# Kernel optimization log

Hardware: AMD Instinct MI355X
Metric: run time of the kernel (lower is better)

## Reference

```python
import jax, jax.numpy as jnp
import numpy as np

N, INC, INN, OUTC, OUTN, MAXD = 16, 32, 65536, 32, 8192, 16

def setup_inputs() -> dict:
    key = jax.random.key(0)
    ks = jax.random.split(key, 7)
    x = jax.random.normal(ks[0], (N, INC, INN), jnp.float32)
    A = jax.random.randint(ks[1], (OUTN, MAXD), 0, INN, dtype=jnp.int64)
    weight = 0.2 * jax.random.normal(ks[2], (INC, INN), jnp.float32)
    # normalize=True with fixed degree MAXD -> mask = 1/maxD everywhere
    mask = jnp.ones((OUTN, MAXD, 1), jnp.float32) / MAXD
    mask_weight = 0.2 * jax.random.normal(ks[3], (OUTN, MAXD, 1), jnp.float32)
    ct_weight = jax.random.normal(ks[4], (OUTC, INC), jnp.float32) / np.sqrt(INC)
    ct_bias = 0.02 * jax.random.normal(ks[5], (OUTC,), jnp.float32)
    bias = 0.2 * jax.random.normal(ks[6], (OUTC, OUTN), jnp.float32)
    return {"x": x, "A": A, "weight": weight, "mask": mask,
            "mask_weight": mask_weight, "ct_weight": ct_weight,
            "ct_bias": ct_bias, "bias": bias}

def reference(x, A, weight, mask, mask_weight, ct_weight, ct_bias, bias):
    n, inc, inn = x.shape
    outn, maxD = A.shape
    # per-input-node channel scaling, then lay out as (inn, N*inc) feature table
    feat = (x * weight).reshape(n * inc, inn).T            # (inn, N*inc)
    emb = feat[A]                                          # (outn, maxD, N*inc) gather
    w = mask_weight * mask                                 # (outn, maxD, 1)
    pooled = (w * emb).reshape(outn, maxD, n, inc).sum(axis=1)  # (outn, N, inc)
    almost_y = jnp.einsum('onc,dc->ond', pooled, ct_weight) + ct_bias  # (outn, N, outc)
    return almost_y.transpose(1, 2, 0) + bias              # (N, outc, outn)
```

## Files before the change

### kernel.cpp

```cpp
#include <hip/hip_runtime.h>
#include <hip/hip_bf16.h>

#define NN    16
#define INC   32
#define INN   65536
#define OUTC  32
#define OUTN  8192
#define MAXD  16
#define NC    512

typedef __attribute__((ext_vector_type(8))) unsigned short ushort8;

__global__ __launch_bounds__(256) void transpose_scale_kernel(
    const float* __restrict__ x,
    const float* __restrict__ weight,
    unsigned short* __restrict__ feat)
{
    __shared__ float tile[64][65];
    const int l  = threadIdx.x;
    const int j0 = blockIdx.x * 64;
    const int r0 = blockIdx.y * 64;

    #pragma unroll
    for (int it = 0; it < 4; ++it) {
        int idx = it * 256 + l;
        int rl  = idx >> 4;
        int jj  = idx & 15;
        int r   = r0 + rl;
        int c   = r & 31;
        int j   = j0 + jj * 4;
        float4 xv = *reinterpret_cast<const float4*>(x + (size_t)r * INN + j);
        float4 wv = *reinterpret_cast<const float4*>(weight + (size_t)c * INN + j);
        tile[jj * 4 + 0][rl] = xv.x * wv.x;
        tile[jj * 4 + 1][rl] = xv.y * wv.y;
        tile[jj * 4 + 2][rl] = xv.z * wv.z;
        tile[jj * 4 + 3][rl] = xv.w * wv.w;
    }
    __syncthreads();

    #pragma unroll
    for (int p = 0; p < 2; ++p) {
        int jl = p * 32 + (l >> 3);
        int rs = (l & 7) * 8;
        ushort8 pk;
        #pragma unroll
        for (int k = 0; k < 8; ++k) {
            float v = tile[jl][rs + k];
            pk[k] = __bfloat16_as_ushort(__float2bfloat16(v));
        }
        *reinterpret_cast<ushort8*>(
            feat + (size_t)(j0 + jl) * NC + r0 + rs) = pk;
    }
}

#define OTILE 16

__global__ __launch_bounds__(256) void gather_gemm_kernel(
    const unsigned short* __restrict__ feat,
    const int*   __restrict__ A,
    const float* __restrict__ mask,
    const float* __restrict__ mw,
    const float* __restrict__ ctw,
    const float* __restrict__ ctb,
    const float* __restrict__ bias,
    float*       __restrict__ out)
{
    __shared__ float pooled[OTILE][NC];
    const int l    = threadIdx.x;
    const int wave = l >> 6;
    const int lane = l & 63;
    const int o0   = blockIdx.x * OTILE;

    const int dout = l & 31;
    float ctr[32];
    #pragma unroll
    for (int q = 0; q < 8; ++q)
        *reinterpret_cast<float4*>(&ctr[4 * q]) =
            *reinterpret_cast<const float4*>(ctw + dout * 32 + 4 * q);
    const float cb = ctb[dout];

    #pragma unroll
    for (int i = 0; i < 4; ++i) {
        const int o  = wave * 4 + i;
        const int oo = o0 + o;
        float acc[8] = {0.f, 0.f, 0.f, 0.f, 0.f, 0.f, 0.f, 0.f};
        #pragma unroll
        for (int d = 0; d < MAXD; ++d) {
            int   j = A[oo * MAXD + d] & (INN - 1);
            float w = mw[oo * MAXD + d] * mask[oo * MAXD + d];
            ushort8 p = *reinterpret_cast<const ushort8*>(
                feat + (size_t)j * NC + lane * 8);
            #pragma unroll
            for (int k = 0; k < 8; ++k)
                acc[k] += w * __uint_as_float((unsigned)p[k] << 16);
        }
        *reinterpret_cast<float4*>(&pooled[o][lane * 8]) =
            make_float4(acc[0], acc[1], acc[2], acc[3]);
        *reinterpret_cast<float4*>(&pooled[o][lane * 8 + 4]) =
            make_float4(acc[4], acc[5], acc[6], acc[7]);
    }
    __syncthreads();

    #pragma unroll
    for (int h = 0; h < 2; ++h) {
        const int n = (l >> 5) + 8 * h;
        float vals[OTILE];
        #pragma unroll
        for (int o = 0; o < OTILE; ++o) {
            float s = cb;
            #pragma unroll
            for (int q = 0; q < 8; ++q) {
                float4 pv = *reinterpret_cast<const float4*>(
                    &pooled[o][n * 32 + 4 * q]);
                s += pv.x * ctr[4 * q + 0] + pv.y * ctr[4 * q + 1]
                   + pv.z * ctr[4 * q + 2] + pv.w * ctr[4 * q + 3];
            }
            vals[o] = s + bias[(size_t)dout * OUTN + o0 + o];
        }
        float4* outp = reinterpret_cast<float4*>(
            out + ((size_t)(n * 32 + dout)) * OUTN + o0);
        #pragma unroll
        for (int q = 0; q < 4; ++q)
            outp[q] = make_float4(vals[4*q], vals[4*q+1], vals[4*q+2], vals[4*q+3]);
    }
}

extern "C" void kernel_launch(void* const* d_in, const int* in_sizes, int n_in,
                              void* d_out, int out_size, void* d_ws, size_t ws_size,
                              hipStream_t stream)
{
    const float* x      = (const float*)d_in[0];
    const int*   A      = (const int*)  d_in[1];
    const float* weight = (const float*)d_in[2];
    const float* mask   = (const float*)d_in[3];
    const float* mw     = (const float*)d_in[4];
    const float* ctw    = (const float*)d_in[5];
    const float* ctb    = (const float*)d_in[6];
    const float* bias   = (const float*)d_in[7];
    float* out = (float*)d_out;

    unsigned short* feat = (unsigned short*)d_ws;

    dim3 gA(INN / 64, NC / 64);
    transpose_scale_kernel<<<gA, 256, 0, stream>>>(x, weight, feat);

    gather_gemm_kernel<<<OUTN / OTILE, 256, 0, stream>>>(
        feat, A, mask, mw, ctw, ctb, bias, out);
}
```

Baseline: 258.7 us.

## Use 512-thread gather blocks with LDS-staged indices, bias, and nontemporal I/O

The gather/GEMM kernel now runs 512 threads per block. Each wave pools two output nodes instead of four, and the neighbour indices, weights and bias tile are staged in LDS. The pooled buffer uses a permuted channel layout so each thread computes all 16 outputs for a single batch row with one pass over ct_weight, and the thread no longer holds 32 ct_weight registers. Nontemporal load/store hints are added for the streaming x reads and the output writes. The aim is more parallelism and fewer redundant global loads, in exchange for an extra barrier and possible LDS bank-conflict changes.

```diff
diff --git a/kernel.cpp b/kernel.cpp
--- a/kernel.cpp
+++ b/kernel.cpp
@@ -10,6 +10,7 @@
 #define NC    512
 
 typedef __attribute__((ext_vector_type(8))) unsigned short ushort8;
+typedef __attribute__((ext_vector_type(4))) float f32x4;
 
 __global__ __launch_bounds__(256) void transpose_scale_kernel(
     const float* __restrict__ x,
@@ -29,12 +30,13 @@
         int r   = r0 + rl;
         int c   = r & 31;
         int j   = j0 + jj * 4;
-        float4 xv = *reinterpret_cast<const float4*>(x + (size_t)r * INN + j);
-        float4 wv = *reinterpret_cast<const float4*>(weight + (size_t)c * INN + j);
-        tile[jj * 4 + 0][rl] = xv.x * wv.x;
-        tile[jj * 4 + 1][rl] = xv.y * wv.y;
-        tile[jj * 4 + 2][rl] = xv.z * wv.z;
-        tile[jj * 4 + 3][rl] = xv.w * wv.w;
+        f32x4 xv = __builtin_nontemporal_load(
+            reinterpret_cast<const f32x4*>(x + (size_t)r * INN + j));
+        f32x4 wv = *reinterpret_cast<const f32x4*>(weight + (size_t)c * INN + j);
+        tile[jj * 4 + 0][rl] = xv[0] * wv[0];
+        tile[jj * 4 + 1][rl] = xv[1] * wv[1];
+        tile[jj * 4 + 2][rl] = xv[2] * wv[2];
+        tile[jj * 4 + 3][rl] = xv[3] * wv[3];
     }
     __syncthreads();
 
@@ -55,7 +57,7 @@
 
 #define OTILE 16
 
-__global__ __launch_bounds__(256) void gather_gemm_kernel(
+__global__ __launch_bounds__(512, 4) void gather_gemm_kernel(
     const unsigned short* __restrict__ feat,
     const int*   __restrict__ A,
     const float* __restrict__ mask,
@@ -66,62 +68,70 @@
     float*       __restrict__ out)
 {
     __shared__ float pooled[OTILE][NC];
+    __shared__ int   A_l[OTILE * MAXD];
+    __shared__ float w_l[OTILE * MAXD];
+    __shared__ float bias_l[32 * OTILE];
+
     const int l    = threadIdx.x;
     const int wave = l >> 6;
     const int lane = l & 63;
     const int o0   = blockIdx.x * OTILE;
 
-    const int dout = l & 31;
-    float ctr[32];
-    #pragma unroll
-    for (int q = 0; q < 8; ++q)
-        *reinterpret_cast<float4*>(&ctr[4 * q]) =
-            *reinterpret_cast<const float4*>(ctw + dout * 32 + 4 * q);
-    const float cb = ctb[dout];
+    if (l < OTILE * MAXD) {
+        A_l[l] = A[o0 * MAXD + l] & (INN - 1);
+        w_l[l] = mw[o0 * MAXD + l] * mask[o0 * MAXD + l];
+    }
+    {
+        int dout = l >> 4, o = l & 15;
+        bias_l[l] = bias[(size_t)dout * OUTN + o0 + o];
+    }
+    __syncthreads();
 
     #pragma unroll
-    for (int i = 0; i < 4; ++i) {
-        const int o  = wave * 4 + i;
-        const int oo = o0 + o;
+    for (int i = 0; i < 2; ++i) {
+        const int o = wave + 8 * i;
         float acc[8] = {0.f, 0.f, 0.f, 0.f, 0.f, 0.f, 0.f, 0.f};
         #pragma unroll
         for (int d = 0; d < MAXD; ++d) {
-            int   j = A[oo * MAXD + d] & (INN - 1);
-            float w = mw[oo * MAXD + d] * mask[oo * MAXD + d];
+            int   j  = A_l[o * MAXD + d];
+            float wv = w_l[o * MAXD + d];
             ushort8 p = *reinterpret_cast<const ushort8*>(
                 feat + (size_t)j * NC + lane * 8);
             #pragma unroll
             for (int k = 0; k < 8; ++k)
-                acc[k] += w * __uint_as_float((unsigned)p[k] << 16);
+                acc[k] += wv * __uint_as_float((unsigned)p[k] << 16);
         }
-        *reinterpret_cast<float4*>(&pooled[o][lane * 8]) =
-            make_float4(acc[0], acc[1], acc[2], acc[3]);
-        *reinterpret_cast<float4*>(&pooled[o][lane * 8 + 4]) =
-            make_float4(acc[4], acc[5], acc[6], acc[7]);
+        *reinterpret_cast<f32x4*>(&pooled[o][lane * 4]) =
+            f32x4{acc[0], acc[1], acc[2], acc[3]};
+        *reinterpret_cast<f32x4*>(&pooled[o][256 + lane * 4]) =
+            f32x4{acc[4], acc[5], acc[6], acc[7]};
     }
     __syncthreads();
 
+    const int dout = l & 31;
+    const int n    = l >> 5;
+    const float cb = ctb[dout];
+    float vals[OTILE];
     #pragma unroll
-    for (int h = 0; h < 2; ++h) {
-        const int n = (l >> 5) + 8 * h;
-        float vals[OTILE];
+    for (int o = 0; o < OTILE; ++o) vals[o] = cb + bias_l[dout * OTILE + o];
+
+    #pragma unroll
+    for (int q = 0; q < 8; ++q) {
+        f32x4 cw = *reinterpret_cast<const f32x4*>(ctw + dout * 32 + 4 * q);
+        const int sbase = (q & 1) * 256 + n * 16 + 4 * (q >> 1);
         #pragma unroll
         for (int o = 0; o < OTILE; ++o) {
-            float s = cb;
-            #pragma unroll
-            for (int q = 0; q < 8; ++q) {
-                float4 pv = *reinterpret_cast<const float4*>(
-                    &pooled[o][n * 32 + 4 * q]);
-                s += pv.x * ctr[4 * q + 0] + pv.y * ctr[4 * q + 1]
-                   + pv.z * ctr[4 * q + 2] + pv.w * ctr[4 * q + 3];
-            }
-            vals[o] = s + bias[(size_t)dout * OUTN + o0 + o];
+            f32x4 pv = *reinterpret_cast<const f32x4*>(&pooled[o][sbase]);
+            vals[o] += pv[0] * cw[0] + pv[1] * cw[1] + pv[2] * cw[2] + pv[3] * cw[3];
         }
-        float4* outp = reinterpret_cast<float4*>(
-            out + ((size_t)(n * 32 + dout)) * OUTN + o0);
-        #pragma unroll
-        for (int q = 0; q < 4; ++q)
-            outp[q] = make_float4(vals[4*q], vals[4*q+1], vals[4*q+2], vals[4*q+3]);
+    }
+
+    float* orow = out + ((size_t)(n * 32 + dout)) * OUTN + o0;
+    #pragma unroll
+    for (int qq = 0; qq < 4; ++qq) {
+        __builtin_nontemporal_store(
+            f32x4{vals[4*qq], vals[4*qq+1], vals[4*qq+2], vals[4*qq+3]},
+            reinterpret_cast<f32x4*>(orow + 4 * qq));
     }
 }
 
@@ -144,6 +154,6 @@
     dim3 gA(INN / 64, NC / 64);
     transpose_scale_kernel<<<gA, 256, 0, stream>>>(x, weight, feat);
 
-    gather_gemm_kernel<<<OUTN / OTILE, 256, 0, stream>>>(
+    gather_gemm_kernel<<<OUTN / OTILE, 512, 0, stream>>>(
         feat, A, mask, mw, ctw, ctb, bias, out);
 }
```

Result: no change. 258.8 us (+0.0%).
